# Kernel tuning notes

Measured on AMD Instinct MI355X. Metric: run time of the kernel, lower is better.

The kernel has to match this reference:

```python
import jax, jax.numpy as jnp
import numpy as np

BLANK = 0          # tf.nn.ctc_loss default blank_index (StringLookup reserves 0 for OOV)
PAD = 127          # padding_value = char_to_num.vocabulary_size()
NEG = -1e30        # log-space 'zero' (avoid -inf to keep grads NaN-free)
B, T, C, L = 1024, 256, 128, 32


def setup_inputs() -> dict:
    key = jax.random.key(0)
    k1, k2 = jax.random.split(key)
    # labels in [1, PAD-1]; none equal PAD so label_length == L (full-length labels)
    y_true = jax.random.randint(k1, (B, L), 1, PAD).astype(jnp.int32)
    y_pred = jax.random.normal(k2, (B, T, C), dtype=jnp.float32)
    return {"y_true": y_true, "y_pred": y_pred}


def _ctc_loss(y_true, y_pred):
    """Faithful jax version of tf.nn.ctc_loss(labels, logits, label_len, T,
    logits_time_major=False, blank_index=0): standard log-space alpha DP."""
    Bn, Tn, Cn = y_pred.shape
    Ln = y_true.shape[1]
    S = 2 * Ln + 1  # extended label length (blanks interleaved)

    logp = jax.nn.log_softmax(y_pred, axis=-1)                    # [B,T,C]

    # extended label sequence: blank, l1, blank, l2, ..., blank   # [B,S]
    ext = jnp.full((Bn, S), BLANK, dtype=y_true.dtype)
    ext = ext.at[:, 1::2].set(y_true)

    # log-probs gathered at extended-label symbols                # [B,T,S]
    lp_ext = jnp.take_along_axis(
        logp, jnp.broadcast_to(ext[:, None, :], (Bn, Tn, S)), axis=2)

    # label_length = count of non-padding entries (mirrors count_nonzero)
    label_len = jnp.sum(y_true != PAD, axis=1)                    # [B]

    # skip transition s-2 -> s allowed iff ext[s] is a non-blank differing
    # from ext[s-2]
    skip_ok = jnp.concatenate(
        [jnp.zeros((Bn, 2), bool),
         (ext[:, 2:] != BLANK) & (ext[:, 2:] != ext[:, :-2])], axis=1)  # [B,S]

    neg1 = jnp.full((Bn, 1), NEG, logp.dtype)
    neg2 = jnp.full((Bn, 2), NEG, logp.dtype)

    alpha0 = jnp.full((Bn, S), NEG, logp.dtype)
    alpha0 = alpha0.at[:, 0].set(lp_ext[:, 0, 0]).at[:, 1].set(lp_ext[:, 0, 1])

    def step(alpha, lp_t):  # alpha,[B,S]  lp_t,[B,S]
        a1 = jnp.concatenate([neg1, alpha[:, :-1]], axis=1)
        a2 = jnp.concatenate([neg2, alpha[:, :-2]], axis=1)
        a2 = jnp.where(skip_ok, a2, NEG)
        new = lp_t + jnp.logaddexp(jnp.logaddexp(alpha, a1), a2)
        return new, None

    lp_seq = jnp.transpose(lp_ext, (1, 0, 2))                     # [T,B,S]
    alphaT, _ = jax.lax.scan(step, alpha0, lp_seq[1:])            # [B,S]

    # total log-likelihood ends at last blank (2*len) or last label (2*len-1)
    bi = jnp.arange(Bn)
    e1 = 2 * label_len
    e2 = 2 * label_len - 1
    loglik = jnp.logaddexp(alphaT[bi, e1], alphaT[bi, e2])        # [B]
    return -loglik


def reference(y_true, y_pred):
    # The original layer returns y_pred and registers the loss via add_loss;
    # the compute-dominant quantity is the per-example CTC loss, returned here.
    return _ctc_loss(y_true, y_pred)
```

## Files before the change

### kernel.cpp

```cpp
#include <hip/hip_runtime.h>
#include <cstdint>


#define CTC_BLANK 0
#define CTC_PAD   127
#define NEG       (-1e30f)

constexpr int Bn = 1024, Tn = 256, Cn = 128, Ln = 32;
constexpr int NSLOT = Ln + 1;

template <int CTRL>
__device__ __forceinline__ float dpp_add(float s) {
    int v = __builtin_amdgcn_update_dpp(0, __float_as_int(s), CTRL, 0xF, 0xF, true);
    return s + __int_as_float(v);
}

__device__ __forceinline__ float dpp_wave_shr1(float src, float old) {
    return __int_as_float(__builtin_amdgcn_update_dpp(
        __float_as_int(old), __float_as_int(src), 0x138, 0xF, 0xF, false));
}

__device__ __forceinline__ float lae2(float a, float b) {
    float m = fmaxf(a, b);
    return m + __logf(__expf(a - m) + __expf(b - m));
}

__global__ __launch_bounds__(256) void ctc_fused_kernel(
        const int*   __restrict__ y_true,
        const float* __restrict__ y_pred,
        float*       __restrict__ out)
{
    __shared__ float Gc[Tn * NSLOT];
    __shared__ int   labels[Ln];
    __shared__ int   cmap[Cn];
    __shared__ int   used[Cn];
    __shared__ int   wcnt[4];
    __shared__ float partS[8];

    const int b    = blockIdx.x;
    const int tid  = threadIdx.x;
    const int lane = tid & 63;
    const int wave = tid >> 6;

    if (tid < Ln) labels[tid] = y_true[b * Ln + tid];
    if (tid < Cn) used[tid] = 0;
    __syncthreads();
    if (tid == 0) used[CTC_BLANK] = 1;
    if (tid < Ln) used[labels[tid]] = 1;
    __syncthreads();
    {
        bool f = (tid < Cn) && (used[tid] != 0);
        unsigned long long m = __ballot(f);
        if (lane == 0) wcnt[wave] = __popcll(m);
        __syncthreads();
        int base = 0;
        for (int w = 0; w < wave; ++w) base += wcnt[w];
        if (tid < Cn)
            cmap[tid] = f ? (base + __popcll(m & ((1ull << lane) - 1ull))) : -1;
        __syncthreads();
    }

    const float* rowbase = y_pred + (size_t)b * Tn * Cn;
    const int half = lane >> 5;
    const int l32  = lane & 31;
    const int4 cm  = ((const int4*)cmap)[l32];
    float acc = 0.f;
    #pragma unroll 8
    for (int it = 0; it < 32; ++it) {
        const int t = it * 8 + wave * 2 + half;
        const float4 v = ((const float4*)(rowbase + t * Cn))[l32];
        if (cm.x >= 0) Gc[t * NSLOT + cm.x] = v.x;
        if (cm.y >= 0) Gc[t * NSLOT + cm.y] = v.y;
        if (cm.z >= 0) Gc[t * NSLOT + cm.z] = v.z;
        if (cm.w >= 0) Gc[t * NSLOT + cm.w] = v.w;
        float s = __expf(v.x) + __expf(v.y) + __expf(v.z) + __expf(v.w);
        s = dpp_add<0x111>(s);
        s = dpp_add<0x112>(s);
        s = dpp_add<0x114>(s);
        s = dpp_add<0x118>(s);
        s = dpp_add<0x142>(s);
        acc += __logf(s);
    }
    if (l32 == 31) partS[wave * 2 + half] = acc;
    __syncthreads();

    if (wave == 0) {
        const int i = lane;
        const bool validO = (i < Ln);
        const bool validE = (i <= Ln);
        const int  myLab   = validO ? labels[i] : -1;
        const int  prevLab = (i >= 1 && i < Ln) ? labels[i - 1] : -1;
        const int  slotO   = validO ? cmap[myLab] : 0;
        const bool skipO   = (i >= 1 && i < Ln) &&
                             (myLab != CTC_BLANK) && (myLab != prevLab);
        const int  len = __popcll(__ballot(validO && (myLab != CTC_PAD)));

        float aE = (i == 0) ? Gc[0]     : NEG;
        float aO = (i == 0) ? Gc[slotO] : NEG;

        float lpB_n = Gc[NSLOT];
        float lpO_n = Gc[NSLOT + slotO];
        for (int t = 1; t < Tn; ++t) {
            const float lpB = lpB_n, lpO = lpO_n;
            const int tn = (t < Tn - 1) ? t + 1 : t;
            lpB_n = Gc[tn * NSLOT];
            lpO_n = Gc[tn * NSLOT + slotO];

            const float aOup = dpp_wave_shr1(aO, NEG);
            const float m  = fmaxf(aE, aOup);
            const float e1 = __expf(aE - m);
            const float e2 = __expf(aOup - m);
            const float sE = e1 + e2;
            const float nE = lpB + m + __logf(sE);
            const float m3 = fmaxf(aO, m);
            const float nO = lpO + m3 +
                __logf(__expf(aO - m3) + (skipO ? sE : e1) * __expf(m - m3));
            aE = validE ? nE : NEG;
            aO = validO ? nO : NEG;
        }

        const float v1 = __shfl(aE, len, 64);
        const float v2 = __shfl(aO, len - 1, 64);
        if (i == 0) {
            const float S = partS[0] + partS[1] + partS[2] + partS[3] +
                            partS[4] + partS[5] + partS[6] + partS[7];
            out[b] = -(lae2(v1, v2) - S);
        }
    }
}

extern "C" void kernel_launch(void* const* d_in, const int* in_sizes, int n_in,
                              void* d_out, int out_size, void* d_ws, size_t ws_size,
                              hipStream_t stream) {
    const int*   y_true = (const int*)d_in[0];
    const float* y_pred = (const float*)d_in[1];
    float*       out    = (float*)d_out;
    ctc_fused_kernel<<<Bn, 256, 0, stream>>>(y_true, y_pred, out);
}
```

Baseline: 228.8 us.

## Split CTC into parallel staging kernel and lightweight 64-thread DP kernel

Replaces the single fused kernel with two launches. The first spreads the log-sum-exp reduction and the gather of used-class logits over 8 time chunks per example, writing compacted logits (pre-scaled to base 2) and partial sums to workspace. The second runs the serial alpha recursion in one 64-thread block per example, using native exp2/log2 instructions. The intent is to stop three idle waves per block from holding resources during the serial DP, which should raise occupancy, at the cost of an extra global round trip (about 34 MB) and a second launch. The fused path is kept as a fallback when the workspace is too small.

```diff
diff --git a/kernel.cpp b/kernel.cpp
--- a/kernel.cpp
+++ b/kernel.cpp
@@ -5,24 +5,187 @@
 #define CTC_BLANK 0
 #define CTC_PAD   127
 #define NEG       (-1e30f)
+#define LOG2E     1.44269504088896340736f
+#define LN2       0.69314718055994530942f
 
 constexpr int Bn = 1024, Tn = 256, Cn = 128, Ln = 32;
 constexpr int NSLOT = Ln + 1;
+constexpr int CHUNK = 32;
+constexpr int NCHUNK = Tn / CHUNK;
+constexpr size_t GC_FLOATS = (size_t)Tn * NSLOT;
+constexpr size_t WS_GC     = (size_t)Bn * GC_FLOATS * 4;
+constexpr size_t WS_S      = (size_t)Bn * NCHUNK * 4;
+constexpr size_t WS_NEEDED = WS_GC + WS_S;
+
+__device__ __forceinline__ float fexp2(float x) { return __builtin_amdgcn_exp2f(x); }
+__device__ __forceinline__ float flog2(float x) { return __builtin_amdgcn_logf(x); }
 
 template <int CTRL>
 __device__ __forceinline__ float dpp_add(float s) {
     int v = __builtin_amdgcn_update_dpp(0, __float_as_int(s), CTRL, 0xF, 0xF, true);
     return s + __int_as_float(v);
 }
-
 __device__ __forceinline__ float dpp_wave_shr1(float src, float old) {
     return __int_as_float(__builtin_amdgcn_update_dpp(
         __float_as_int(old), __float_as_int(src), 0x138, 0xF, 0xF, false));
 }
-
 __device__ __forceinline__ float lae2(float a, float b) {
     float m = fmaxf(a, b);
     return m + __logf(__expf(a - m) + __expf(b - m));
+}
+
+__global__ __launch_bounds__(256) void ctc_stage_kernel(
+        const int*   __restrict__ y_true,
+        const float* __restrict__ y_pred,
+        float*       __restrict__ gws,
+        float*       __restrict__ sws)
+{
+    __shared__ float Gt[CHUNK * NSLOT];
+    __shared__ int   labels[Ln];
+    __shared__ int   cmap[Cn];
+    __shared__ int   used[Cn];
+    __shared__ int   wcnt[4];
+    __shared__ float partS[8];
+
+    const int chunk = blockIdx.x;
+    const int b     = blockIdx.y;
+    const int tid   = threadIdx.x;
+    const int lane  = tid & 63;
+    const int wave  = tid >> 6;
+
+    if (tid < Ln) labels[tid] = y_true[b * Ln + tid];
+    if (tid < Cn) used[tid] = 0;
+    __syncthreads();
+    if (tid == 0) used[CTC_BLANK] = 1;
+    if (tid < Ln) used[labels[tid]] = 1;
+    __syncthreads();
+    {
+        bool f = (tid < Cn) && (used[tid] != 0);
+        unsigned long long m = __ballot(f);
+        if (lane == 0) wcnt[wave] = __popcll(m);
+        __syncthreads();
+        int base = 0;
+        for (int w = 0; w < wave; ++w) base += wcnt[w];
+        if (tid < Cn)
+            cmap[tid] = f ? (base + __popcll(m & ((1ull << lane) - 1ull))) : -1;
+        __syncthreads();
+    }
+
+    const float* rowbase = y_pred + ((size_t)b * Tn + chunk * CHUNK) * Cn;
+    const int half = lane >> 5;
+    const int l32  = lane & 31;
+    const int4 cm  = ((const int4*)cmap)[l32];
+    float acc = 0.f;
+    #pragma unroll
+    for (int k = 0; k < 4; ++k) {
+        const int r = k * 8 + wave * 2 + half;
+        const float4 v = ((const float4*)(rowbase + r * Cn))[l32];
+        if (cm.x >= 0) Gt[r * NSLOT + cm.x] = v.x * LOG2E;
+        if (cm.y >= 0) Gt[r * NSLOT + cm.y] = v.y * LOG2E;
+        if (cm.z >= 0) Gt[r * NSLOT + cm.z] = v.z * LOG2E;
+        if (cm.w >= 0) Gt[r * NSLOT + cm.w] = v.w * LOG2E;
+        float s = __expf(v.x) + __expf(v.y) + __expf(v.z) + __expf(v.w);
+        s = dpp_add<0x111>(s);
+        s = dpp_add<0x112>(s);
+        s = dpp_add<0x114>(s);
+        s = dpp_add<0x118>(s);
+        s = dpp_add<0x142>(s);
+        acc += __logf(s);
+    }
+    if (l32 == 31) partS[wave * 2 + half] = acc;
+    __syncthreads();
+
+    float4*       dst = (float4*)(gws + (size_t)b * GC_FLOATS +
+                                  (size_t)chunk * (CHUNK * NSLOT));
+    const float4* src = (const float4*)Gt;
+    dst[tid] = src[tid];
+    if (tid < 8) dst[256 + tid] = src[256 + tid];
+    if (tid == 0)
+        sws[b * NCHUNK + chunk] = partS[0] + partS[1] + partS[2] + partS[3] +
+                                  partS[4] + partS[5] + partS[6] + partS[7];
+}
+
+__global__ __launch_bounds__(64) void ctc_dp_kernel(
+        const int*   __restrict__ y_true,
+        const float* __restrict__ gws,
+        const float* __restrict__ sws,
+        float*       __restrict__ out)
+{
+    __shared__ __align__(16) float Gc[GC_FLOATS];
+    __shared__ int labels[Ln];
+    __shared__ int used[Cn];
+    __shared__ int cmap[Cn];
+
+    const int b    = blockIdx.x;
+    const int lane = threadIdx.x;
+
+    {
+        const float4* src = (const float4*)(gws + (size_t)b * GC_FLOATS);
+        float4*       dst = (float4*)Gc;
+        #pragma unroll
+        for (int k = 0; k < 33; ++k) dst[k * 64 + lane] = src[k * 64 + lane];
+    }
+
+    if (lane < Ln) labels[lane] = y_true[b * Ln + lane];
+    used[lane] = 0; used[64 + lane] = 0;
+    __syncthreads();
+    if (lane == 0) used[CTC_BLANK] = 1;
+    if (lane < Ln) used[labels[lane]] = 1;
+    __syncthreads();
+    {
+        const unsigned long long below = (1ull << lane) - 1ull;
+        const unsigned long long m0 = __ballot(used[lane] != 0);
+        const unsigned long long m1 = __ballot(used[64 + lane] != 0);
+        cmap[lane]      = used[lane]      ? (int)__popcll(m0 & below) : -1;
+        cmap[64 + lane] = used[64 + lane] ? (int)(__popcll(m0) +
+                                                  __popcll(m1 & below)) : -1;
+    }
+    __syncthreads();
+
+    const int  i      = lane;
+    const bool validO = (i < Ln);
+    const bool validE = (i <= Ln);
+    const int  myLab   = validO ? labels[i] : -1;
+    const int  prevLab = (i >= 1 && i < Ln) ? labels[i - 1] : -1;
+    const int  slotO   = validO ? cmap[myLab] : 0;
+    const bool skipO   = (i >= 1 && i < Ln) &&
+                         (myLab != CTC_BLANK) && (myLab != prevLab);
+    const int  len = __popcll(__ballot(validO && (myLab != CTC_PAD)));
+
+    float aE = (i == 0) ? Gc[0]     : NEG;
+    float aO = (i == 0) ? Gc[slotO] : NEG;
+
+    float lpB_n = Gc[NSLOT];
+    float lpO_n = Gc[NSLOT + slotO];
+    for (int t = 1; t < Tn; ++t) {
+        const float lpB = lpB_n, lpO = lpO_n;
+        const int tn = (t < Tn - 1) ? t + 1 : t;
+        lpB_n = Gc[tn * NSLOT];
+        lpO_n = Gc[tn * NSLOT + slotO];
+
+        const float aOup = dpp_wave_shr1(aO, NEG);
+        const float m  = fmaxf(aE, aOup);
+        const float e1 = fexp2(aE - m);
+        const float e2 = fexp2(aOup - m);
+        const float sE = e1 + e2;
+        const float nE = lpB + m + flog2(sE);
+        const float m3 = fmaxf(aO, m);
+        const float nO = lpO + m3 +
+            flog2(fexp2(aO - m3) + (skipO ? sE : e1) * fexp2(m - m3));
+        aE = validE ? nE : NEG;
+        aO = validO ? nO : NEG;
+    }
+
+    const float v1 = __shfl(aE, len, 64);
+    const float v2 = __shfl(aO, len - 1, 64);
+    if (i == 0) {
+        float S = 0.f;
+        #pragma unroll
+        for (int j = 0; j < NCHUNK; ++j) S += sws[b * NCHUNK + j];
+        const float mm = fmaxf(v1, v2);
+        const float L2 = mm + flog2(fexp2(v1 - mm) + fexp2(v2 - mm));
+        out[b] = S - LN2 * L2;
+    }
 }
 
 __global__ __launch_bounds__(256) void ctc_fused_kernel(
@@ -97,7 +260,6 @@
 
         float aE = (i == 0) ? Gc[0]     : NEG;
         float aO = (i == 0) ? Gc[slotO] : NEG;
-
         float lpB_n = Gc[NSLOT];
         float lpO_n = Gc[NSLOT + slotO];
         for (int t = 1; t < Tn; ++t) {
@@ -105,7 +267,6 @@
             const int tn = (t < Tn - 1) ? t + 1 : t;
             lpB_n = Gc[tn * NSLOT];
             lpO_n = Gc[tn * NSLOT + slotO];
-
             const float aOup = dpp_wave_shr1(aO, NEG);
             const float m  = fmaxf(aE, aOup);
             const float e1 = __expf(aE - m);
@@ -118,7 +279,6 @@
             aE = validE ? nE : NEG;
             aO = validO ? nO : NEG;
         }
-
         const float v1 = __shfl(aE, len, 64);
         const float v2 = __shfl(aO, len - 1, 64);
         if (i == 0) {
@@ -135,5 +295,12 @@
     const int*   y_true = (const int*)d_in[0];
     const float* y_pred = (const float*)d_in[1];
     float*       out    = (float*)d_out;
-    ctc_fused_kernel<<<Bn, 256, 0, stream>>>(y_true, y_pred, out);
-}
+    if (ws_size >= WS_NEEDED) {
+        float* gws = (float*)d_ws;
+        float* sws = (float*)d_ws + (size_t)Bn * GC_FLOATS;
+        ctc_stage_kernel<<<dim3(NCHUNK, Bn), 256, 0, stream>>>(y_true, y_pred, gws, sws);
+        ctc_dp_kernel<<<Bn, 64, 0, stream>>>(y_true, gws, sws, out);
+    } else {
+        ctc_fused_kernel<<<Bn, 256, 0, stream>>>(y_true, y_pred, out);
+    }
+}
```

After: 219.4 us. -4.1%, faster.

## Store gathered logits as fp16 in log2 domain, double-buffer loads, prefetch DP inputs

Applied to the files above, without the earlier changes.

The gathered per-slot logits are pre-scaled by log2(e) and stored in LDS as fp16, which halves the shared-memory footprint so more blocks can share a CU; launch bounds now request 4 blocks per SM. The logsumexp pass loads 8 rows per group into a double buffer so global loads overlap the exp/reduce work. The serial alpha recursion runs in base 2 using native exp2/log2 intrinsics and reads its inputs through a 4-deep register prefetch queue, converting back with ln2 at the end. The fp16 storage lowers the precision of the logits summed over 256 steps, which could push the result past a tight tolerance.

```diff
diff --git a/kernel.cpp b/kernel.cpp
--- a/kernel.cpp
+++ b/kernel.cpp
@@ -5,34 +5,34 @@
 #define CTC_BLANK 0
 #define CTC_PAD   127
 #define NEG       (-1e30f)
+#define LOG2E     1.44269504088896340736f
+#define LN2       0.69314718055994530942f
 
 constexpr int Bn = 1024, Tn = 256, Cn = 128, Ln = 32;
 constexpr int NSLOT = Ln + 1;
+constexpr int PF = 4;
+
+__device__ __forceinline__ float fexp2(float x) { return __builtin_amdgcn_exp2f(x); }
+__device__ __forceinline__ float flog2(float x) { return __builtin_amdgcn_logf(x); }
 
 template <int CTRL>
 __device__ __forceinline__ float dpp_add(float s) {
     int v = __builtin_amdgcn_update_dpp(0, __float_as_int(s), CTRL, 0xF, 0xF, true);
     return s + __int_as_float(v);
 }
-
 __device__ __forceinline__ float dpp_wave_shr1(float src, float old) {
     return __int_as_float(__builtin_amdgcn_update_dpp(
         __float_as_int(old), __float_as_int(src), 0x138, 0xF, 0xF, false));
 }
 
-__device__ __forceinline__ float lae2(float a, float b) {
-    float m = fmaxf(a, b);
-    return m + __logf(__expf(a - m) + __expf(b - m));
-}
-
-__global__ __launch_bounds__(256) void ctc_fused_kernel(
+__global__ __launch_bounds__(256, 4) void ctc_fused_kernel(
         const int*   __restrict__ y_true,
         const float* __restrict__ y_pred,
         float*       __restrict__ out)
 {
-    __shared__ float Gc[Tn * NSLOT];
+    __shared__ _Float16 Gc[Tn * NSLOT];
     __shared__ int   labels[Ln];
-    __shared__ int   cmap[Cn];
+    __shared__ __align__(16) int cmap[Cn];
     __shared__ int   used[Cn];
     __shared__ int   wcnt[4];
     __shared__ float partS[8];
@@ -65,21 +65,37 @@
     const int l32  = lane & 31;
     const int4 cm  = ((const int4*)cmap)[l32];
     float acc = 0.f;
-    #pragma unroll 8
-    for (int it = 0; it < 32; ++it) {
-        const int t = it * 8 + wave * 2 + half;
-        const float4 v = ((const float4*)(rowbase + t * Cn))[l32];
-        if (cm.x >= 0) Gc[t * NSLOT + cm.x] = v.x;
-        if (cm.y >= 0) Gc[t * NSLOT + cm.y] = v.y;
-        if (cm.z >= 0) Gc[t * NSLOT + cm.z] = v.z;
-        if (cm.w >= 0) Gc[t * NSLOT + cm.w] = v.w;
-        float s = __expf(v.x) + __expf(v.y) + __expf(v.z) + __expf(v.w);
-        s = dpp_add<0x111>(s);
-        s = dpp_add<0x112>(s);
-        s = dpp_add<0x114>(s);
-        s = dpp_add<0x118>(s);
-        s = dpp_add<0x142>(s);
-        acc += __logf(s);
+
+    float4 v[2][8];
+    #pragma unroll
+    for (int j = 0; j < 8; ++j) {
+        const int r = (wave * 4 + 0) * 16 + j * 2 + half;
+        v[0][j] = ((const float4*)(rowbase + r * Cn))[l32];
+    }
+    for (int g = 0; g < 4; ++g) {
+        if (g < 3) {
+            #pragma unroll
+            for (int j = 0; j < 8; ++j) {
+                const int r = (wave * 4 + g + 1) * 16 + j * 2 + half;
+                v[(g + 1) & 1][j] = ((const float4*)(rowbase + r * Cn))[l32];
+            }
+        }
+        #pragma unroll
+        for (int j = 0; j < 8; ++j) {
+            const float4 x = v[g & 1][j];
+            const int r = (wave * 4 + g) * 16 + j * 2 + half;
+            if (cm.x >= 0) Gc[r * NSLOT + cm.x] = (_Float16)(x.x * LOG2E);
+            if (cm.y >= 0) Gc[r * NSLOT + cm.y] = (_Float16)(x.y * LOG2E);
+            if (cm.z >= 0) Gc[r * NSLOT + cm.z] = (_Float16)(x.z * LOG2E);
+            if (cm.w >= 0) Gc[r * NSLOT + cm.w] = (_Float16)(x.w * LOG2E);
+            float s = __expf(x.x) + __expf(x.y) + __expf(x.z) + __expf(x.w);
+            s = dpp_add<0x111>(s);
+            s = dpp_add<0x112>(s);
+            s = dpp_add<0x114>(s);
+            s = dpp_add<0x118>(s);
+            s = dpp_add<0x142>(s);
+            acc += __logf(s);
+        }
     }
     if (l32 == 31) partS[wave * 2 + half] = acc;
     __syncthreads();
@@ -95,26 +111,34 @@
                              (myLab != CTC_BLANK) && (myLab != prevLab);
         const int  len = __popcll(__ballot(validO && (myLab != CTC_PAD)));
 
-        float aE = (i == 0) ? Gc[0]     : NEG;
-        float aO = (i == 0) ? Gc[slotO] : NEG;
+        float aE = (i == 0) ? (float)Gc[0]     : NEG;
+        float aO = (i == 0) ? (float)Gc[slotO] : NEG;
 
-        float lpB_n = Gc[NSLOT];
-        float lpO_n = Gc[NSLOT + slotO];
+        float pB[PF], pO[PF];
+        #pragma unroll
+        for (int j = 0; j < PF; ++j) {
+            const int tj = 1 + j;
+            pB[j] = (float)Gc[tj * NSLOT];
+            pO[j] = (float)Gc[tj * NSLOT + slotO];
+        }
+        #pragma unroll 4
         for (int t = 1; t < Tn; ++t) {
-            const float lpB = lpB_n, lpO = lpO_n;
-            const int tn = (t < Tn - 1) ? t + 1 : t;
-            lpB_n = Gc[tn * NSLOT];
-            lpO_n = Gc[tn * NSLOT + slotO];
+            const float lpB = pB[0], lpO = pO[0];
+            #pragma unroll
+            for (int j = 0; j < PF - 1; ++j) { pB[j] = pB[j + 1]; pO[j] = pO[j + 1]; }
+            const int tn = (t + PF < Tn) ? t + PF : Tn - 1;
+            pB[PF - 1] = (float)Gc[tn * NSLOT];
+            pO[PF - 1] = (float)Gc[tn * NSLOT + slotO];
 
             const float aOup = dpp_wave_shr1(aO, NEG);
             const float m  = fmaxf(aE, aOup);
-            const float e1 = __expf(aE - m);
-            const float e2 = __expf(aOup - m);
+            const float e1 = fexp2(aE - m);
+            const float e2 = fexp2(aOup - m);
             const float sE = e1 + e2;
-            const float nE = lpB + m + __logf(sE);
+            const float nE = lpB + m + flog2(sE);
             const float m3 = fmaxf(aO, m);
             const float nO = lpO + m3 +
-                __logf(__expf(aO - m3) + (skipO ? sE : e1) * __expf(m - m3));
+                flog2(fexp2(aO - m3) + (skipO ? sE : e1) * fexp2(m - m3));
             aE = validE ? nE : NEG;
             aO = validO ? nO : NEG;
         }
@@ -124,7 +148,9 @@
         if (i == 0) {
             const float S = partS[0] + partS[1] + partS[2] + partS[3] +
                             partS[4] + partS[5] + partS[6] + partS[7];
-            out[b] = -(lae2(v1, v2) - S);
+            const float mm = fmaxf(v1, v2);
+            const float L2 = mm + flog2(fexp2(v1 - mm) + fexp2(v2 - mm));
+            out[b] = S - LN2 * L2;
         }
     }
 }
```

After: 220.2 us. 3.8% less time.
